# Kernel tuning notes

Measured on AMD Instinct MI355X. Metric: run time of the kernel, lower is better.

## Reference

```python
import jax, jax.numpy as jnp
import numpy as np

K = 16          # neighbors (init kwarg k)
LEAK = 0.2      # LeakyReLU slope
EPS = 1e-5      # GroupNorm eps
GROUPS = 4


def knn_idx(coor_k, coor_q, k):
    # coor_* : (B, 3, N); returns (B, Nq, k) indices of k nearest keys per query
    qk = jnp.einsum('bdq,bdk->bqk', coor_q, coor_k)
    q2 = jnp.sum(coor_q * coor_q, axis=1)[:, :, None]
    k2 = jnp.sum(coor_k * coor_k, axis=1)[:, None, :]
    d2 = q2 + k2 - 2.0 * qk                     # (B, Nq, Nk) squared distances
    _, idx = jax.lax.top_k(-d2, k)
    return idx


def gather_feats(x_k, idx):
    # x_k (B, D, Nk), idx (B, Nq, k) -> (B, D, Nq, k)
    feat = jax.vmap(lambda fk, i: fk[i])(jnp.transpose(x_k, (0, 2, 1)), idx)  # (B,Nq,k,D)
    return jnp.transpose(feat, (0, 3, 1, 2))


def graph_feature(coor_q, x_q, coor_k, x_k, k):
    idx = knn_idx(coor_k, coor_q, k)
    feat = gather_feats(x_k, idx)                # (B, D, Nq, k)
    xq = x_q[:, :, :, None]
    return jnp.concatenate([feat - xq, jnp.broadcast_to(xq, feat.shape)], axis=1)


def group_norm(x, gamma, beta):
    B, C, N, Kk = x.shape
    xg = x.reshape(B, GROUPS, C // GROUPS, N, Kk)
    mu = xg.mean(axis=(2, 3, 4), keepdims=True)
    var = xg.var(axis=(2, 3, 4), keepdims=True)
    xn = ((xg - mu) * jax.lax.rsqrt(var + EPS)).reshape(B, C, N, Kk)
    return xn * gamma[None, :, None, None] + beta[None, :, None, None]


def conv_gn_lrelu(x, w, gamma, beta):
    y = jnp.einsum('oc,bcnk->bonk', w, x)        # 1x1 conv, no bias
    y = group_norm(y, gamma, beta)
    return jnp.where(y > 0, y, LEAK * y)


def fps(xyz, npoint):
    # xyz (B, N, 3) -> (B, npoint) farthest-point-sampling indices, start at 0
    B, N, _ = xyz.shape
    d0 = jnp.full((B, N), 1e10, dtype=xyz.dtype)

    def step(carry, _):
        dist, far = carry
        centroid = jnp.take_along_axis(xyz, far[:, None, None], axis=1)  # (B,1,3)
        d = jnp.sum((xyz - centroid) ** 2, axis=-1)
        dist = jnp.minimum(dist, d)
        nxt = jnp.argmax(dist, axis=-1).astype(jnp.int32)
        return (dist, nxt), far

    far0 = jnp.zeros((B,), dtype=jnp.int32)
    _, idxs = jax.lax.scan(step, (d0, far0), None, length=npoint)
    return jnp.transpose(idxs)                   # (B, npoint)


def fps_downsample(coor, x, num_group):
    # coor (B,3,N), x (B,D,N)
    fidx = fps(jnp.transpose(coor, (0, 2, 1)), num_group)   # (B, num_group)
    comb = jnp.concatenate([coor, x], axis=1)                # (B, 3+D, N)
    new = jax.vmap(lambda c, i: c[:, i])(comb, fidx)         # (B, 3+D, num_group)
    return new[:, :3], new[:, 3:]


def setup_inputs() -> dict:
    key = jax.random.key(0)
    ks = jax.random.split(key, 8)
    B, N = 16, 2048
    return {
        'x': jax.random.normal(ks[0], (B, N, 3), jnp.float32),
        'num0': 512,
        'num1': 128,
        'w_in': jax.random.normal(ks[1], (8, 3), jnp.float32) * 0.3,
        'b_in': jax.random.normal(ks[2], (8,), jnp.float32) * 0.1,
        'w1': jax.random.normal(ks[3], (32, 16), jnp.float32) * 0.2,
        'g1': jnp.ones((32,), jnp.float32), 'be1': jnp.zeros((32,), jnp.float32),
        'w2': jax.random.normal(ks[4], (64, 64), jnp.float32) * 0.12,
        'g2': jnp.ones((64,), jnp.float32), 'be2': jnp.zeros((64,), jnp.float32),
        'w3': jax.random.normal(ks[5], (64, 128), jnp.float32) * 0.09,
        'g3': jnp.ones((64,), jnp.float32), 'be3': jnp.zeros((64,), jnp.float32),
        'w4': jax.random.normal(ks[6], (128, 128), jnp.float32) * 0.09,
        'g4': jnp.ones((128,), jnp.float32), 'be4': jnp.zeros((128,), jnp.float32),
    }


def reference(x, num0, num1, w_in, b_in, w1, g1, be1, w2, g2, be2,
              w3, g3, be3, w4, g4, be4):
    coor = jnp.transpose(x, (0, 2, 1))                       # (B,3,N)
    f = jnp.einsum('oc,bcn->bon', w_in, coor) + b_in[None, :, None]  # (B,8,N)

    f = graph_feature(coor, f, coor, f, K)                   # (B,16,N,K)
    f = conv_gn_lrelu(f, w1, g1, be1).max(axis=-1)           # (B,32,N)

    coor_q, f_q = fps_downsample(coor, f, num0)
    f = graph_feature(coor_q, f_q, coor, f, K)               # (B,64,num0,K)
    f = conv_gn_lrelu(f, w2, g2, be2).max(axis=-1)           # (B,64,num0)
    coor = coor_q

    f = graph_feature(coor, f, coor, f, K)                   # (B,128,num0,K)
    f = conv_gn_lrelu(f, w3, g3, be3).max(axis=-1)           # (B,64,num0)

    coor_q, f_q = fps_downsample(coor, f, num1)
    f = graph_feature(coor_q, f_q, coor, f, K)               # (B,128,num1,K)
    f = conv_gn_lrelu(f, w4, g4, be4).max(axis=-1)           # (B,128,num1)

    return jnp.transpose(coor_q, (0, 2, 1)), jnp.transpose(f, (0, 2, 1))
```

## Files before the change

kernel.cpp:

```cpp
#include <hip/hip_runtime.h>

#define KNN 16
static constexpr int BB = 16;
static constexpr float LEAK = 0.2f;
static constexpr float EPSV = 1e-5f;
typedef unsigned long long u64;

__device__ __forceinline__ void ce_asc(u64 &a, u64 &b) {
  u64 x = a, y = b; bool sw = y < x; a = sw ? y : x; b = sw ? x : y;
}
__device__ __forceinline__ void ce_desc(u64 &a, u64 &b) {
  u64 x = a, y = b; bool sw = x < y; a = sw ? y : x; b = sw ? x : y;
}
__device__ __forceinline__ void bitonic_sort16(u64 *T) {
#pragma unroll
  for (int k = 2; k <= 16; k <<= 1) {
#pragma unroll
    for (int j = k >> 1; j > 0; j >>= 1) {
#pragma unroll
      for (int i = 0; i < 16; ++i) {
        int l = i ^ j;
        if (l > i) {
          if ((i & k) == 0) ce_asc(T[i], T[l]); else ce_desc(T[i], T[l]);
        }
      }
    }
  }
}
__device__ __forceinline__ void merge_sorted16(u64 *R, const u64 *T) {
#pragma unroll
  for (int i = 0; i < 16; ++i) {
    u64 t = T[15 - i];
    R[i] = t < R[i] ? t : R[i];
  }
#pragma unroll
  for (int j = 8; j > 0; j >>= 1) {
#pragma unroll
    for (int i = 0; i < 16; ++i) {
      int l = i ^ j;
      if (l > i) ce_asc(R[i], R[l]);
    }
  }
}
template<int KC>
__device__ __forceinline__ void merge_row(const u64* __restrict__ p, u64* R) {
#pragma unroll
  for (int s = 0; s < 16; ++s) R[s] = p[s];
#pragma unroll
  for (int c = 1; c < KC; ++c) {
    u64 T[16];
#pragma unroll
    for (int s = 0; s < 16; ++s) T[s] = p[(size_t)c*KNN + s];
    merge_sorted16(R, T);
  }
}

__device__ __forceinline__ void f0_dev(const float* __restrict__ x,
    const float* __restrict__ w_in, const float* __restrict__ b_in,
    float* __restrict__ f0, int bid) {
  int i = bid * 256 + threadIdx.x;
  float px = x[i*3+0], py = x[i*3+1], pz = x[i*3+2];
#pragma unroll
  for (int o = 0; o < 8; ++o) {
    f0[i*8+o] = w_in[o*3+0]*px + w_in[o*3+1]*py + w_in[o*3+2]*pz + b_in[o];
  }
}

__device__ void knn_part_dev(const float* __restrict__ qxyz, int Nq,
    const float* __restrict__ kxyz, int Nk, int KC, u64* __restrict__ part,
    char* sm, int bid) {
  float4* keys = (float4*)sm;
  int nqb = (Nq + 255) >> 8;
  int c  = bid % KC;
  int qb = (bid / KC) % nqb;
  int b  = bid / (KC * nqb);
  int nkc = Nk / KC;
  int kbase = c * nkc;
  for (int j = threadIdx.x; j < nkc; j += 256) {
    const float* kp = kxyz + (size_t)(b*Nk + kbase + j)*3;
    float kx = kp[0], ky = kp[1], kz = kp[2];
    keys[j] = make_float4(kx, ky, kz, kx*kx + ky*ky + kz*kz);
  }
  __syncthreads();
  int q = (qb << 8) + threadIdx.x;
  if (q >= Nq) return;
  const float* qp = qxyz + (size_t)(b*Nq + q)*3;
  float qx = qp[0], qy = qp[1], qz = qp[2];
  float q2 = qx*qx + qy*qy + qz*qz;
  u64 R[16];
#pragma unroll
  for (int s = 0; s < 16; ++s) R[s] = 0xFFFFFFFFFFFFFFFFull;
  for (int j0 = 0; j0 < nkc; j0 += 16) {
    u64 T[16];
#pragma unroll
    for (int u = 0; u < 16; ++u) {
      float4 kk = keys[j0 + u];
      float qk = qx*kk.x + qy*kk.y + qz*kk.z;
      float d2 = q2 + kk.w - 2.0f*qk;
      int bb = __float_as_int(d2);
      unsigned k32 = (unsigned)bb ^ (unsigned)((bb >> 31) | 0x80000000);
      T[u] = ((u64)k32 << 32) | (unsigned)(kbase + j0 + u);
    }
    bitonic_sort16(T);
    merge_sorted16(R, T);
  }
  u64* op = part + ((size_t)(b*Nq + q)*KC + c)*KNN;
#pragma unroll
  for (int s = 0; s < KNN; ++s) op[s] = R[s];
}

__device__ __forceinline__ u64 fps_max64(u64 a, u64 b) { return a > b ? a : b; }
template<int CTRL>
__device__ __forceinline__ float fps_dpp_fmax(float v) {
  int nb = __builtin_amdgcn_update_dpp(0, __float_as_int(v), CTRL, 0xF, 0xF, false);
  return fmaxf(v, __int_as_float(nb));
}
__device__ __forceinline__ float rl_f(float v, int l) {
  return __int_as_float(__builtin_amdgcn_readlane(__float_as_int(v), l));
}
template<int P, bool SAVE>
__device__ void fps_seg_dev(const float* __restrict__ xyz, int np,
    int t0, int t1, int* __restrict__ fidx,
    float* __restrict__ g_dl, int* __restrict__ g_far,
    float* __restrict__ cq, char* sm, int b) {
  constexpr int NN = P * 256;
  float4* sc  = (float4*)sm;
  int* s_fid  = (int*)(sm + NN*16);
  u64* s_key  = (u64*)(sm + NN*16 + 2048);
  __builtin_amdgcn_s_setprio(1);
  int tid = threadIdx.x;
  int w = tid >> 6, lw = tid & 63;
  float px[P], py[P], pz[P], dl[P];
#pragma unroll
  for (int i = 0; i < P; ++i) {
    int p = tid * P + i;
    const float* pp = xyz + (size_t)(b*NN + p)*3;
    px[i] = pp[0]; py[i] = pp[1]; pz[i] = pp[2];
    sc[p] = make_float4(px[i], py[i], pz[i], 0.f);
  }
  int far;
  if (t0 == 0) {
#pragma unroll
    for (int i = 0; i < P; ++i) dl[i] = 1e10f;
    far = 0;
  } else {
#pragma unroll
    for (int i = 0; i < P; ++i) dl[i] = g_dl[b*NN + tid*P + i];
    far = g_far[b];
  }
  __syncthreads();
  for (int t = t0; t < t1; ++t) {
    if (tid == 0) s_fid[t] = far;
    float4 cc = sc[far];
#pragma unroll
    for (int i = 0; i < P; ++i) {
      float dx = __fsub_rn(px[i], cc.x);
      float dy = __fsub_rn(py[i], cc.y);
      float dz = __fsub_rn(pz[i], cc.z);
      float d = __fadd_rn(__fadd_rn(__fmul_rn(dx,dx), __fmul_rn(dy,dy)), __fmul_rn(dz,dz));
      dl[i] = fminf(dl[i], d);
    }
    float m[P];
#pragma unroll
    for (int i = 0; i < P; ++i) m[i] = dl[i];
#pragma unroll
    for (int st = P/2; st > 0; st >>= 1) {
#pragma unroll
      for (int i = 0; i < P; ++i) if (i < st) m[i] = fmaxf(m[i], m[i + st]);
    }
    float lmax = m[0];
    unsigned msk = 0u;
#pragma unroll
    for (int i = 0; i < P; ++i) msk |= (dl[i] == lmax) ? (1u << i) : 0u;
    int lidx = tid * P + __builtin_ctz(msk);
    float v = lmax;
    v = fps_dpp_fmax<0x111>(v);
    v = fps_dpp_fmax<0x112>(v);
    v = fps_dpp_fmax<0x114>(v);
    v = fps_dpp_fmax<0x118>(v);
    v = fps_dpp_fmax<0x142>(v);
    v = fps_dpp_fmax<0x143>(v);
    float wmax = rl_f(v, 63);
    u64 bal = __ballot(lmax == wmax);
    int l0 = __ffsll((unsigned long long)bal) - 1;
    int wp = __builtin_amdgcn_readlane(lidx, l0);
    int buf = t & 1;
    if (lw == 0)
      s_key[buf*4 + w] = ((u64)__float_as_uint(wmax) << 32) | (unsigned)(~wp);
    __syncthreads();
    u64 best = s_key[buf*4 + 0];
    best = fps_max64(best, s_key[buf*4 + 1]);
    best = fps_max64(best, s_key[buf*4 + 2]);
    best = fps_max64(best, s_key[buf*4 + 3]);
    far = (int)(~(unsigned)(best & 0xFFFFFFFFull));
  }
  for (int t = t0 + tid; t < t1; t += 256) fidx[b*np + t] = s_fid[t];
  if constexpr (SAVE) {
#pragma unroll
    for (int i = 0; i < P; ++i) g_dl[b*NN + tid*P + i] = dl[i];
    if (tid == 0) g_far[b] = far;
  } else {
    for (int j = tid; j < np; j += 256) {
      int p = (j >= t0) ? s_fid[j] : fidx[b*np + j];
      float4 c = sc[p];
      float* cp = cq + (size_t)(b*np + j)*3;
      cp[0] = c.x; cp[1] = c.y; cp[2] = c.z;
    }
  }
  __builtin_amdgcn_s_setprio(0);
}

template<int P, bool SAVE>
__device__ void fps2_wave_dev(const float* __restrict__ xyz, int np,
    int t0, int t1, int* __restrict__ fidx,
    float* __restrict__ g_dl, int* __restrict__ g_far,
    float* __restrict__ cq, char* sm, int b) {
  constexpr int NN = P * 64;
  int* s_fid = (int*)sm;
  __builtin_amdgcn_s_setprio(1);
  int l = threadIdx.x;
  float px[P], py[P], pz[P], dl[P];
#pragma unroll
  for (int i = 0; i < P; ++i) {
    int p = l * P + i;
    const float* pp = xyz + (size_t)(b*NN + p)*3;
    px[i] = pp[0]; py[i] = pp[1]; pz[i] = pp[2];
  }
  int far;
  if (t0 == 0) {
#pragma unroll
    for (int i = 0; i < P; ++i) dl[i] = 1e10f;
    far = 0;
  } else {
#pragma unroll
    for (int i = 0; i < P; ++i) dl[i] = g_dl[b*NN + l*P + i];
    far = g_far[b];
  }
  const float* fp = xyz + (size_t)(b*NN + far)*3;
  float ccx = fp[0], ccy = fp[1], ccz = fp[2];
  for (int t = t0; t < t1; ++t) {
    if (l == 0) s_fid[t] = far;
#pragma unroll
    for (int i = 0; i < P; ++i) {
      float dx = __fsub_rn(px[i], ccx);
      float dy = __fsub_rn(py[i], ccy);
      float dz = __fsub_rn(pz[i], ccz);
      float d = __fadd_rn(__fadd_rn(__fmul_rn(dx,dx), __fmul_rn(dy,dy)), __fmul_rn(dz,dz));
      dl[i] = fminf(dl[i], d);
    }
    float m[P];
#pragma unroll
    for (int i = 0; i < P; ++i) m[i] = dl[i];
#pragma unroll
    for (int st = P/2; st > 0; st >>= 1) {
#pragma unroll
      for (int i = 0; i < P; ++i) if (i < st) m[i] = fmaxf(m[i], m[i + st]);
    }
    float lmax = m[0];
    unsigned msk = 0u;
#pragma unroll
    for (int i = 0; i < P; ++i) msk |= (dl[i] == lmax) ? (1u << i) : 0u;
    int ib = __builtin_ctz(msk);
    int lidx = l * P + ib;
    float cxl = px[P-1], cyl = py[P-1], czl = pz[P-1];
#pragma unroll
    for (int i = P-1; i >= 0; --i) {
      bool tk = (msk >> i) & 1u;
      cxl = tk ? px[i] : cxl;
      cyl = tk ? py[i] : cyl;
      czl = tk ? pz[i] : czl;
    }
    float v = lmax;
    v = fps_dpp_fmax<0x111>(v);
    v = fps_dpp_fmax<0x112>(v);
    v = fps_dpp_fmax<0x114>(v);
    v = fps_dpp_fmax<0x118>(v);
    v = fps_dpp_fmax<0x142>(v);
    v = fps_dpp_fmax<0x143>(v);
    float wmax = rl_f(v, 63);
    u64 bal = __ballot(lmax == wmax);
    int l0 = __ffsll((unsigned long long)bal) - 1;
    far = __builtin_amdgcn_readlane(lidx, l0);
    ccx = rl_f(cxl, l0); ccy = rl_f(cyl, l0); ccz = rl_f(czl, l0);
  }
  for (int t = t0 + l; t < t1; t += 64) fidx[b*np + t] = s_fid[t];
  if constexpr (SAVE) {
#pragma unroll
    for (int i = 0; i < P; ++i) g_dl[b*NN + l*P + i] = dl[i];
    if (l == 0) g_far[b] = far;
  } else {
    for (int j = l; j < np; j += 64) {
      int p = (j >= t0) ? s_fid[j] : fidx[b*np + j];
      const float* sp = xyz + (size_t)(b*NN + p)*3;
      float* cp = cq + (size_t)(b*np + j)*3;
      cp[0] = sp[0]; cp[1] = sp[1]; cp[2] = sp[2];
    }
  }
  __builtin_amdgcn_s_setprio(0);
}

template<int C, int O, int QB, int KC, int NB>
__device__ void conv_dev(const float* __restrict__ fsrc, int Nsrc,
    const float* __restrict__ fq, int Nfq, const int* __restrict__ qmap,
    int Nq, const u64* __restrict__ part,
    const float* __restrict__ w, float* __restrict__ ym, float* __restrict__ yn,
    double2* __restrict__ pp1, char* sm, int bid) {
  constexpr int Og = O / 4;
  constexpr int C4 = C / 4;
  double* rs  = (double*)sm;
  double* rs2 = rs + 256;
  float* ft   = (float*)(sm + 4096);
  float* fqs  = ft + QB*KNN*C;
  int* s_idx  = (int*)(fqs + QB*C);
  int tid = threadIdx.x;
  int chunk = bid % NB;
  int b = bid / NB;
  int q0 = chunk * QB;
  if (tid < QB) {
    const u64* p = part + (size_t)(b*Nq + q0 + tid)*KC*KNN;
    u64 R[16];
    merge_row<KC>(p, R);
#pragma unroll
    for (int s = 0; s < 16; ++s) s_idx[tid*KNN + s] = (int)(unsigned)(R[s] & 0xFFFFFFFFu);
  } else if (tid >= 64 && tid < 64 + QB*C4) {
    int t = tid - 64;
    int ql = t / C4, c4 = t % C4;
    int q = q0 + ql;
    int sq = qmap ? qmap[b*Nq + q] : q;
    ((float4*)&fqs[ql*C])[c4] = ((const float4*)(fq + ((size_t)b*Nfq + sq)*C))[c4];
  }
  __syncthreads();
  for (int v = tid; v < QB*KNN*C4; v += 256) {
    int row = v / C4, c4 = v % C4;
    int ql = row / KNN, k = row % KNN;
    int src = s_idx[ql*KNN + k];
    ((float4*)&ft[(ql*KNN + k)*C])[c4] = ((const float4*)(fsrc + (size_t)(b*Nsrc + src)*C))[c4];
  }
  __syncthreads();
  int ql = tid / O, o = tid % O;
  float4 wr4[C4];
  float bs = 0.f;
  const float4* wp4 = (const float4*)(w + (size_t)o*2*C);
#pragma unroll
  for (int c4 = 0; c4 < C4; ++c4) {
    float4 lo = wp4[c4], hi = wp4[C4 + c4];
    float4 fv = ((const float4*)&fqs[ql*C])[c4];
    bs += (hi.x - lo.x) * fv.x;
    bs += (hi.y - lo.y) * fv.y;
    bs += (hi.z - lo.z) * fv.z;
    bs += (hi.w - lo.w) * fv.w;
    wr4[c4] = lo;
  }
  float mx = -3.4e38f, mn = 3.4e38f;
  double s = 0.0, s2 = 0.0;
  for (int k = 0; k < KNN; ++k) {
    float acc = bs;
    const float4* fv = (const float4*)&ft[(ql*KNN + k)*C];
#pragma unroll
    for (int c4 = 0; c4 < C4; ++c4) {
      float4 v = fv[c4];
      acc += wr4[c4].x*v.x; acc += wr4[c4].y*v.y;
      acc += wr4[c4].z*v.z; acc += wr4[c4].w*v.w;
    }
    mx = fmaxf(mx, acc);
    mn = fminf(mn, acc);
    s += acc;
    s2 += (double)acc * (double)acc;
  }
  size_t oidx = (size_t)(b*Nq + q0 + ql)*O + o;
  ym[oidx] = mx;
  yn[oidx] = mn;
  rs[tid] = s; rs2[tid] = s2;
  __syncthreads();
#pragma unroll
  for (int st = QB/2; st > 0; st >>= 1) {
    if (ql < st) { rs[tid] += rs[tid + st*O]; rs2[tid] += rs2[tid + st*O]; }
    __syncthreads();
  }
#pragma unroll
  for (int st = Og/2; st > 0; st >>= 1) {
    if (tid < O && (o % Og) < st) { rs[tid] += rs[tid + st]; rs2[tid] += rs2[tid + st]; }
    __syncthreads();
  }
  if (tid < O && (o % Og) == 0) {
    int g = o / Og;
    pp1[((size_t)b*NB + chunk)*4 + g] = make_double2(rs[tid], rs2[tid]);
  }
}

template<int O, int NB, int FCH, int NQ>
__device__ void fin_dev(const float* __restrict__ ym, const float* __restrict__ yn,
    const double2* __restrict__ pp1, const float* __restrict__ gamma,
    const float* __restrict__ beta, float* __restrict__ fout, char* sm, int bid) {
  constexpr int Og = O / 4;
  double* red  = (double*)sm;
  double* red2 = red + 64;
  float* s_mu  = (float*)(red2 + 64);
  float* s_rsv = s_mu + 4;
  int tid = threadIdx.x;
  int b = bid / FCH;
  int f = bid % FCH;
  if (tid < 64) {
    int g = tid >> 4, j = tid & 15;
    double s = 0.0, s2 = 0.0;
    for (int c = j; c < NB; c += 16) {
      double2 v = pp1[((size_t)b*NB + c)*4 + g];
      s += v.x; s2 += v.y;
    }
    red[tid] = s; red2[tid] = s2;
  }
  __syncthreads();
#pragma unroll
  for (int st = 8; st > 0; st >>= 1) {
    if (tid < 64 && (tid & 15) < st) { red[tid] += red[tid+st]; red2[tid] += red2[tid+st]; }
    __syncthreads();
  }
  if (tid < 4) {
    double cnt = (double)Og * (double)NQ * (double)KNN;
    double mu = red[tid*16] / cnt;
    double var = red2[tid*16] / cnt - mu*mu;
    s_mu[tid] = (float)mu;
    s_rsv[tid] = 1.0f / sqrtf((float)var + EPSV);
  }
  __syncthreads();
  constexpr int PER = NQ * O / FCH;
  int e0 = f * PER;
  for (int e = e0 + tid; e < e0 + PER; e += 256) {
    int q = e / O, o = e % O;
    int g = o / Og;
    size_t idx = (size_t)(b*NQ + q)*O + o;
    float ga = gamma[o], be = beta[o];
    float ysel = (ga >= 0.f) ? ym[idx] : yn[idx];
    float xn = (ysel - s_mu[g]) * s_rsv[g];
    float yv = xn*ga + be;
    yv = yv > 0.f ? yv : LEAK*yv;
    fout[idx] = yv;
  }
}

__global__ __launch_bounds__(256) void fusedA_kernel(const float* __restrict__ x,
    const float* __restrict__ w_in, const float* __restrict__ b_in,
    float* __restrict__ f0, u64* __restrict__ part, int* __restrict__ fidx1,
    float* __restrict__ g_dl, int* __restrict__ g_far) {
  extern __shared__ char sm[];
  int bid = blockIdx.x;
  if (bid < 16)        fps_seg_dev<8,true>(x, 512, 0, 280, fidx1, g_dl, g_far, nullptr, sm, bid);
  else if (bid < 1040) knn_part_dev(x, 2048, x, 2048, 8, part, sm, bid - 16);
  else                 f0_dev(x, w_in, b_in, f0, bid - 1040);
}

__global__ __launch_bounds__(256) void conv1_kernel(const float* __restrict__ x,
    int* __restrict__ fidx1, float* __restrict__ g_dl, int* __restrict__ g_far,
    const float* __restrict__ f0, const u64* __restrict__ part,
    const float* __restrict__ w1, float* __restrict__ ym, float* __restrict__ yn,
    double2* __restrict__ pp1) {
  extern __shared__ char sm[];
  int bid = blockIdx.x;
  if (bid < 16) fps_seg_dev<8,true>(x, 512, 280, 460, fidx1, g_dl, g_far, nullptr, sm, bid);
  else          conv_dev<8,32,8,8,256>(f0, 2048, f0, 2048, nullptr, 2048, part, w1, ym, yn, pp1, sm, bid - 16);
}

__global__ __launch_bounds__(256) void fin1_kernel(const float* __restrict__ x,
    int* __restrict__ fidx1, float* __restrict__ g_dl, int* __restrict__ g_far,
    float* __restrict__ cq1,
    const float* __restrict__ ym, const float* __restrict__ yn,
    const double2* __restrict__ pp1, const float* __restrict__ g1,
    const float* __restrict__ be1, float* __restrict__ f1) {
  extern __shared__ char sm[];
  int bid = blockIdx.x;
  if (bid < 16) fps_seg_dev<8,false>(x, 512, 460, 512, fidx1, g_dl, g_far, cq1, sm, bid);
  else          fin_dev<32,256,32,2048>(ym, yn, pp1, g1, be1, f1, sm, bid - 16);
}

__global__ __launch_bounds__(256) void fusedB_kernel(const float* __restrict__ cq1,
    const float* __restrict__ x, u64* __restrict__ part2, u64* __restrict__ part3,
    int* __restrict__ fidx2, float* __restrict__ g_dl, int* __restrict__ g_far) {
  extern __shared__ char sm[];
  int bid = blockIdx.x;
  if (bid < 16) {
    if (threadIdx.x < 64)
      fps2_wave_dev<8,true>(cq1, 128, 0, 100, fidx2, g_dl, g_far, nullptr, sm, bid);
  } else if (bid < 272) {
    knn_part_dev(cq1, 512, x, 2048, 8, part2, sm, bid - 16);
  } else {
    knn_part_dev(cq1, 512, cq1, 512, 8, part3, sm, bid - 272);
  }
}

__global__ __launch_bounds__(256) void conv2_kernel(const float* __restrict__ cq1,
    int* __restrict__ fidx2, float* __restrict__ g_dl, int* __restrict__ g_far,
    float* __restrict__ cq2,
    const float* __restrict__ f1, const int* __restrict__ fidx1,
    const u64* __restrict__ part2, const float* __restrict__ w2,
    float* __restrict__ ym, float* __restrict__ yn, double2* __restrict__ pp1) {
  extern __shared__ char sm[];
  int bid = blockIdx.x;
  if (bid < 16) {
    if (threadIdx.x < 64)
      fps2_wave_dev<8,false>(cq1, 128, 100, 128, fidx2, g_dl, g_far, cq2, sm, bid);
  }
  else conv_dev<32,64,4,8,128>(f1, 2048, f1, 2048, fidx1, 512, part2, w2, ym, yn, pp1, sm, bid - 16);
}

__global__ __launch_bounds__(256) void fin2_kernel(const float* __restrict__ ym,
    const float* __restrict__ yn, const double2* __restrict__ pp1,
    const float* __restrict__ g2, const float* __restrict__ be2,
    float* __restrict__ f2) {
  extern __shared__ char sm[];
  fin_dev<64,128,16,512>(ym, yn, pp1, g2, be2, f2, sm, blockIdx.x);
}

__global__ __launch_bounds__(256) void conv3k4_kernel(const float* __restrict__ cq2,
    const float* __restrict__ cq1, u64* __restrict__ part4,
    const float* __restrict__ f2, const u64* __restrict__ part3,
    const float* __restrict__ w3, float* __restrict__ ym, float* __restrict__ yn,
    double2* __restrict__ pp1) {
  extern __shared__ char sm[];
  int bid = blockIdx.x;
  if (bid < 128) knn_part_dev(cq2, 128, cq1, 512, 8, part4, sm, bid);
  else           conv_dev<64,64,4,8,128>(f2, 512, f2, 512, nullptr, 512, part3, w3, ym, yn, pp1, sm, bid - 128);
}

__global__ __launch_bounds__(256) void fin3_kernel(const float* __restrict__ ym,
    const float* __restrict__ yn, const double2* __restrict__ pp1,
    const float* __restrict__ g3, const float* __restrict__ be3,
    float* __restrict__ f3) {
  extern __shared__ char sm[];
  fin_dev<64,128,16,512>(ym, yn, pp1, g3, be3, f3, sm, blockIdx.x);
}

__global__ __launch_bounds__(256) void conv4_kernel(const float* __restrict__ f3,
    const int* __restrict__ fidx2, const u64* __restrict__ part4,
    const float* __restrict__ w4, float* __restrict__ ym, float* __restrict__ yn,
    double2* __restrict__ pp1) {
  extern __shared__ char sm[];
  conv_dev<64,128,2,8,64>(f3, 512, f3, 512, fidx2, 128, part4, w4, ym, yn, pp1, sm, blockIdx.x);
}

__global__ __launch_bounds__(256) void fin4_kernel(const float* __restrict__ ym,
    const float* __restrict__ yn, const double2* __restrict__ pp1,
    const float* __restrict__ g4, const float* __restrict__ be4,
    float* __restrict__ f4) {
  extern __shared__ char sm[];
  fin_dev<128,64,8,128>(ym, yn, pp1, g4, be4, f4, sm, blockIdx.x);
}

extern "C" void kernel_launch(void* const* d_in, const int* in_sizes, int n_in,
                              void* d_out, int out_size, void* d_ws, size_t ws_size,
                              hipStream_t stream) {
  const float* x    = (const float*)d_in[0];
  const float* w_in = (const float*)d_in[3];
  const float* b_in = (const float*)d_in[4];
  const float* w1 = (const float*)d_in[5];
  const float* g1 = (const float*)d_in[6];
  const float* be1= (const float*)d_in[7];
  const float* w2 = (const float*)d_in[8];
  const float* g2 = (const float*)d_in[9];
  const float* be2= (const float*)d_in[10];
  const float* w3 = (const float*)d_in[11];
  const float* g3 = (const float*)d_in[12];
  const float* be3= (const float*)d_in[13];
  const float* w4 = (const float*)d_in[14];
  const float* g4 = (const float*)d_in[15];
  const float* be4= (const float*)d_in[16];
  float* out = (float*)d_out;
  (void)in_sizes; (void)n_in; (void)out_size; (void)ws_size;

  char* ws = (char*)d_ws;
  size_t off = 0;
  auto alloc = [&](size_t count) {
    void* p = ws + off;
    off += (count * 4 + 255) & ~(size_t)255;
    return p;
  };
  float* f0    = (float*)alloc(16*2048*8);
  float* f1    = (float*)alloc(16*2048*32);
  float* f2    = (float*)alloc(16*512*64);
  float* f3    = (float*)alloc(16*512*64);
  float* cq1   = (float*)alloc(16*512*3);
  float* ym    = (float*)alloc(16*2048*32);
  float* yn    = (float*)alloc(16*2048*32);
  double2* pp1 = (double2*)alloc(16*256*4*4);
  int* fidx1   = (int*)alloc(16*512);
  int* fidx2   = (int*)alloc(16*128);
  float* g_dl1 = (float*)alloc(16*2048);
  int* g_far1  = (int*)alloc(16);
  float* g_dl2 = (float*)alloc(16*512);
  int* g_far2  = (int*)alloc(16);
  u64* part1 = (u64*)alloc((size_t)2 * 16*2048*8*16);
  u64* part2 = part1;
  u64* part3 = part1 + (size_t)16*512*8*16;
  u64* part4 = part1 + (size_t)2*16*512*8*16;

  float* cq2 = out;
  float* f4  = out + 16*128*3;

  constexpr size_t SM_F1  = 2048*16 + 2048 + 64;
  constexpr size_t SM_F2W = 512;
  constexpr size_t SM_KNN = 4096;
  constexpr size_t SM_C1  = 4096 + 8*KNN*8*4 + 8*8*4 + 8*KNN*4;
  constexpr size_t SM_C2  = 4096 + 4*KNN*32*4 + 4*32*4 + 4*KNN*4;
  constexpr size_t SM_C3  = 4096 + 4*KNN*64*4 + 4*64*4 + 4*KNN*4;
  constexpr size_t SM_C4  = 4096 + 2*KNN*64*4 + 2*64*4 + 2*KNN*4;
  constexpr size_t SM_FIN = 1056;
  auto mx2 = [](size_t a, size_t b) { return a > b ? a : b; };

  fusedA_kernel<<<1168, 256, mx2(SM_F1, SM_KNN), stream>>>(x, w_in, b_in, f0, part1, fidx1, g_dl1, g_far1);
  conv1_kernel<<<4112, 256, mx2(SM_F1, SM_C1), stream>>>(x, fidx1, g_dl1, g_far1, f0, part1, w1, ym, yn, pp1);
  fin1_kernel<<<528, 256, mx2(SM_F1, SM_FIN), stream>>>(x, fidx1, g_dl1, g_far1, cq1, ym, yn, pp1, g1, be1, f1);

  fusedB_kernel<<<528, 256, mx2(SM_F2W, SM_KNN), stream>>>(cq1, x, part2, part3, fidx2, g_dl2, g_far2);
  conv2_kernel<<<2064, 256, mx2(SM_F2W, SM_C2), stream>>>(cq1, fidx2, g_dl2, g_far2, cq2, f1, fidx1, part2, w2, ym, yn, pp1);
  fin2_kernel<<<256, 256, SM_FIN, stream>>>(ym, yn, pp1, g2, be2, f2);

  conv3k4_kernel<<<2176, 256, mx2(SM_KNN, SM_C3), stream>>>(cq2, cq1, part4, f2, part3, w3, ym, yn, pp1);
  fin3_kernel<<<256, 256, SM_FIN, stream>>>(ym, yn, pp1, g3, be3, f3);

  conv4_kernel<<<1024, 256, SM_C4, stream>>>(f3, fidx2, part4, w4, ym, yn, pp1);
  fin4_kernel<<<128, 256, SM_FIN, stream>>>(ym, yn, pp1, g4, be4, f4);
}
```

Before: 479.3 us.

## Reuse full-set KNN partials for subsampled queries and drop a launch

Since FPS-selected queries are a subset of the key set, the KNN partial lists for stages 2 and 4 are now read from the existing full-set partials (part1 and part3) indexed through the FPS map, instead of being recomputed. This removes the separate query-vs-full KNN passes, which lets fusedB be folded into conv2 and the second FPS run unsplit in one wave. The conv3 kernel loses its KNN blocks. The change depends on the self-KNN results matching the query-KNN results exactly, and the FPS on 512 points now sits serially inside conv2 with no split across launches.

```diff
diff --git a/kernel.cpp b/kernel.cpp
--- a/kernel.cpp
+++ b/kernel.cpp
@@ -210,11 +210,9 @@
   __builtin_amdgcn_s_setprio(0);
 }
 
-template<int P, bool SAVE>
+template<int P>
 __device__ void fps2_wave_dev(const float* __restrict__ xyz, int np,
-    int t0, int t1, int* __restrict__ fidx,
-    float* __restrict__ g_dl, int* __restrict__ g_far,
-    float* __restrict__ cq, char* sm, int b) {
+    int* __restrict__ fidx, float* __restrict__ cq, char* sm, int b) {
   constexpr int NN = P * 64;
   int* s_fid = (int*)sm;
   __builtin_amdgcn_s_setprio(1);
@@ -225,20 +223,12 @@
     int p = l * P + i;
     const float* pp = xyz + (size_t)(b*NN + p)*3;
     px[i] = pp[0]; py[i] = pp[1]; pz[i] = pp[2];
-  }
-  int far;
-  if (t0 == 0) {
-#pragma unroll
-    for (int i = 0; i < P; ++i) dl[i] = 1e10f;
-    far = 0;
-  } else {
-#pragma unroll
-    for (int i = 0; i < P; ++i) dl[i] = g_dl[b*NN + l*P + i];
-    far = g_far[b];
-  }
-  const float* fp = xyz + (size_t)(b*NN + far)*3;
+    dl[i] = 1e10f;
+  }
+  int far = 0;
+  const float* fp = xyz + (size_t)(b*NN)*3;
   float ccx = fp[0], ccy = fp[1], ccz = fp[2];
-  for (int t = t0; t < t1; ++t) {
+  for (int t = 0; t < np; ++t) {
     if (l == 0) s_fid[t] = far;
 #pragma unroll
     for (int i = 0; i < P; ++i) {
@@ -283,26 +273,19 @@
     far = __builtin_amdgcn_readlane(lidx, l0);
     ccx = rl_f(cxl, l0); ccy = rl_f(cyl, l0); ccz = rl_f(czl, l0);
   }
-  for (int t = t0 + l; t < t1; t += 64) fidx[b*np + t] = s_fid[t];
-  if constexpr (SAVE) {
-#pragma unroll
-    for (int i = 0; i < P; ++i) g_dl[b*NN + l*P + i] = dl[i];
-    if (l == 0) g_far[b] = far;
-  } else {
-    for (int j = l; j < np; j += 64) {
-      int p = (j >= t0) ? s_fid[j] : fidx[b*np + j];
-      const float* sp = xyz + (size_t)(b*NN + p)*3;
-      float* cp = cq + (size_t)(b*np + j)*3;
-      cp[0] = sp[0]; cp[1] = sp[1]; cp[2] = sp[2];
-    }
+  for (int t = l; t < np; t += 64) {
+    int p = s_fid[t];
+    fidx[b*np + t] = p;
+    const float* sp = xyz + (size_t)(b*NN + p)*3;
+    float* cp = cq + (size_t)(b*np + t)*3;
+    cp[0] = sp[0]; cp[1] = sp[1]; cp[2] = sp[2];
   }
   __builtin_amdgcn_s_setprio(0);
 }
 
 template<int C, int O, int QB, int KC, int NB>
 __device__ void conv_dev(const float* __restrict__ fsrc, int Nsrc,
-    const float* __restrict__ fq, int Nfq, const int* __restrict__ qmap,
-    int Nq, const u64* __restrict__ part,
+    const int* __restrict__ qmap, int Nq, const u64* __restrict__ part,
     const float* __restrict__ w, float* __restrict__ ym, float* __restrict__ yn,
     double2* __restrict__ pp1, char* sm, int bid) {
   constexpr int Og = O / 4;
@@ -317,7 +300,9 @@
   int b = bid / NB;
   int q0 = chunk * QB;
   if (tid < QB) {
-    const u64* p = part + (size_t)(b*Nq + q0 + tid)*KC*KNN;
+    int q = q0 + tid;
+    int sq = qmap ? qmap[b*Nq + q] : q;
+    const u64* p = part + ((size_t)b*Nsrc + sq)*KC*KNN;
     u64 R[16];
     merge_row<KC>(p, R);
 #pragma unroll
@@ -327,7 +312,7 @@
     int ql = t / C4, c4 = t % C4;
     int q = q0 + ql;
     int sq = qmap ? qmap[b*Nq + q] : q;
-    ((float4*)&fqs[ql*C])[c4] = ((const float4*)(fq + ((size_t)b*Nfq + sq)*C))[c4];
+    ((float4*)&fqs[ql*C])[c4] = ((const float4*)(fsrc + ((size_t)b*Nsrc + sq)*C))[c4];
   }
   __syncthreads();
   for (int v = tid; v < QB*KNN*C4; v += 256) {
@@ -457,7 +442,7 @@
   extern __shared__ char sm[];
   int bid = blockIdx.x;
   if (bid < 16) fps_seg_dev<8,true>(x, 512, 280, 460, fidx1, g_dl, g_far, nullptr, sm, bid);
-  else          conv_dev<8,32,8,8,256>(f0, 2048, f0, 2048, nullptr, 2048, part, w1, ym, yn, pp1, sm, bid - 16);
+  else          conv_dev<8,32,8,8,256>(f0, 2048, nullptr, 2048, part, w1, ym, yn, pp1, sm, bid - 16);
 }
 
 __global__ __launch_bounds__(256) void fin1_kernel(const float* __restrict__ x,
@@ -472,34 +457,21 @@
   else          fin_dev<32,256,32,2048>(ym, yn, pp1, g1, be1, f1, sm, bid - 16);
 }
 
-__global__ __launch_bounds__(256) void fusedB_kernel(const float* __restrict__ cq1,
-    const float* __restrict__ x, u64* __restrict__ part2, u64* __restrict__ part3,
-    int* __restrict__ fidx2, float* __restrict__ g_dl, int* __restrict__ g_far) {
+__global__ __launch_bounds__(256) void conv2_kernel(const float* __restrict__ cq1,
+    int* __restrict__ fidx2, float* __restrict__ cq2, u64* __restrict__ part3,
+    const float* __restrict__ f1, const int* __restrict__ fidx1,
+    const u64* __restrict__ part1, const float* __restrict__ w2,
+    float* __restrict__ ym, float* __restrict__ yn, double2* __restrict__ pp1) {
   extern __shared__ char sm[];
   int bid = blockIdx.x;
   if (bid < 16) {
     if (threadIdx.x < 64)
-      fps2_wave_dev<8,true>(cq1, 128, 0, 100, fidx2, g_dl, g_far, nullptr, sm, bid);
+      fps2_wave_dev<8>(cq1, 128, fidx2, cq2, sm, bid);
   } else if (bid < 272) {
-    knn_part_dev(cq1, 512, x, 2048, 8, part2, sm, bid - 16);
+    knn_part_dev(cq1, 512, cq1, 512, 8, part3, sm, bid - 16);
   } else {
-    knn_part_dev(cq1, 512, cq1, 512, 8, part3, sm, bid - 272);
-  }
-}
-
-__global__ __launch_bounds__(256) void conv2_kernel(const float* __restrict__ cq1,
-    int* __restrict__ fidx2, float* __restrict__ g_dl, int* __restrict__ g_far,
-    float* __restrict__ cq2,
-    const float* __restrict__ f1, const int* __restrict__ fidx1,
-    const u64* __restrict__ part2, const float* __restrict__ w2,
-    float* __restrict__ ym, float* __restrict__ yn, double2* __restrict__ pp1) {
-  extern __shared__ char sm[];
-  int bid = blockIdx.x;
-  if (bid < 16) {
-    if (threadIdx.x < 64)
-      fps2_wave_dev<8,false>(cq1, 128, 100, 128, fidx2, g_dl, g_far, cq2, sm, bid);
-  }
-  else conv_dev<32,64,4,8,128>(f1, 2048, f1, 2048, fidx1, 512, part2, w2, ym, yn, pp1, sm, bid - 16);
+    conv_dev<32,64,4,8,128>(f1, 2048, fidx1, 512, part1, w2, ym, yn, pp1, sm, bid - 272);
+  }
 }
 
 __global__ __launch_bounds__(256) void fin2_kernel(const float* __restrict__ ym,
@@ -510,15 +482,11 @@
   fin_dev<64,128,16,512>(ym, yn, pp1, g2, be2, f2, sm, blockIdx.x);
 }
 
-__global__ __launch_bounds__(256) void conv3k4_kernel(const float* __restrict__ cq2,
-    const float* __restrict__ cq1, u64* __restrict__ part4,
-    const float* __restrict__ f2, const u64* __restrict__ part3,
-    const float* __restrict__ w3, float* __restrict__ ym, float* __restrict__ yn,
-    double2* __restrict__ pp1) {
-  extern __shared__ char sm[];
-  int bid = blockIdx.x;
-  if (bid < 128) knn_part_dev(cq2, 128, cq1, 512, 8, part4, sm, bid);
-  else           conv_dev<64,64,4,8,128>(f2, 512, f2, 512, nullptr, 512, part3, w3, ym, yn, pp1, sm, bid - 128);
+__global__ __launch_bounds__(256) void conv3_kernel(const float* __restrict__ f2,
+    const u64* __restrict__ part3, const float* __restrict__ w3,
+    float* __restrict__ ym, float* __restrict__ yn, double2* __restrict__ pp1) {
+  extern __shared__ char sm[];
+  conv_dev<64,64,4,8,128>(f2, 512, nullptr, 512, part3, w3, ym, yn, pp1, sm, blockIdx.x);
 }
 
 __global__ __launch_bounds__(256) void fin3_kernel(const float* __restrict__ ym,
@@ -530,11 +498,11 @@
 }
 
 __global__ __launch_bounds__(256) void conv4_kernel(const float* __restrict__ f3,
-    const int* __restrict__ fidx2, const u64* __restrict__ part4,
+    const int* __restrict__ fidx2, const u64* __restrict__ part3,
     const float* __restrict__ w4, float* __restrict__ ym, float* __restrict__ yn,
     double2* __restrict__ pp1) {
   extern __shared__ char sm[];
-  conv_dev<64,128,2,8,64>(f3, 512, f3, 512, fidx2, 128, part4, w4, ym, yn, pp1, sm, blockIdx.x);
+  conv_dev<64,128,2,8,64>(f3, 512, fidx2, 128, part3, w4, ym, yn, pp1, sm, blockIdx.x);
 }
 
 __global__ __launch_bounds__(256) void fin4_kernel(const float* __restrict__ ym,
@@ -585,12 +553,8 @@
   int* fidx2   = (int*)alloc(16*128);
   float* g_dl1 = (float*)alloc(16*2048);
   int* g_far1  = (int*)alloc(16);
-  float* g_dl2 = (float*)alloc(16*512);
-  int* g_far2  = (int*)alloc(16);
   u64* part1 = (u64*)alloc((size_t)2 * 16*2048*8*16);
-  u64* part2 = part1;
-  u64* part3 = part1 + (size_t)16*512*8*16;
-  u64* part4 = part1 + (size_t)2*16*512*8*16;
+  u64* part3 = (u64*)alloc((size_t)2 * 16*512*8*16);
 
   float* cq2 = out;
   float* f4  = out + 16*128*3;
@@ -604,18 +568,19 @@
   constexpr size_t SM_C4  = 4096 + 2*KNN*64*4 + 2*64*4 + 2*KNN*4;
   constexpr size_t SM_FIN = 1056;
   auto mx2 = [](size_t a, size_t b) { return a > b ? a : b; };
+  auto mx3 = [&](size_t a, size_t b, size_t c) { return mx2(a, mx2(b, c)); };
 
   fusedA_kernel<<<1168, 256, mx2(SM_F1, SM_KNN), stream>>>(x, w_in, b_in, f0, part1, fidx1, g_dl1, g_far1);
   conv1_kernel<<<4112, 256, mx2(SM_F1, SM_C1), stream>>>(x, fidx1, g_dl1, g_far1, f0, part1, w1, ym, yn, pp1);
   fin1_kernel<<<528, 256, mx2(SM_F1, SM_FIN), stream>>>(x, fidx1, g_dl1, g_far1, cq1, ym, yn, pp1, g1, be1, f1);
 
-  fusedB_kernel<<<528, 256, mx2(SM_F2W, SM_KNN), stream>>>(cq1, x, part2, part3, fidx2, g_dl2, g_far2);
-  conv2_kernel<<<2064, 256, mx2(SM_F2W, SM_C2), stream>>>(cq1, fidx2, g_dl2, g_far2, cq2, f1, fidx1, part2, w2, ym, yn, pp1);
+  conv2_kernel<<<2320, 256, mx3(SM_F2W, SM_KNN, SM_C2), stream>>>(cq1, fidx2, cq2, part3,
+      f1, fidx1, part1, w2, ym, yn, pp1);
   fin2_kernel<<<256, 256, SM_FIN, stream>>>(ym, yn, pp1, g2, be2, f2);
 
-  conv3k4_kernel<<<2176, 256, mx2(SM_KNN, SM_C3), stream>>>(cq2, cq1, part4, f2, part3, w3, ym, yn, pp1);
+  conv3_kernel<<<2048, 256, SM_C3, stream>>>(f2, part3, w3, ym, yn, pp1);
   fin3_kernel<<<256, 256, SM_FIN, stream>>>(ym, yn, pp1, g3, be3, f3);
 
-  conv4_kernel<<<1024, 256, SM_C4, stream>>>(f3, fidx2, part4, w4, ym, yn, pp1);
+  conv4_kernel<<<1024, 256, SM_C4, stream>>>(f3, fidx2, part3, w4, ym, yn, pp1);
   fin4_kernel<<<128, 256, SM_FIN, stream>>>(ym, yn, pp1, g4, be4, f4);
 }
```

Result: faster. 428.3 us (-10.6%).
